# Performance work log

Measured on AMD Instinct MI355X. Metric: run time of the kernel, lower is better.

Reference implementation:

```python
import jax, jax.numpy as jnp
import numpy as np

D = 1024
H = 16
DK = D // H


def apply_rope(x):
    # x: [B, H, T, dk]; interleaved-pair RoPE as in the torch source
    T, dim = x.shape[-2], x.shape[-1]
    inv_freq = 1.0 / (10000.0 ** (jnp.arange(0, dim, 2, dtype=x.dtype) / dim))  # [dk/2]
    pos = jnp.arange(T, dtype=x.dtype)
    sinusoid = pos[:, None] * inv_freq[None, :]  # [T, dk/2]
    sin, cos = jnp.sin(sinusoid), jnp.cos(sinusoid)
    x1, x2 = x[..., ::2], x[..., 1::2]
    rot = jnp.stack([x1 * cos - x2 * sin, x1 * sin + x2 * cos], axis=-1)
    return rot.reshape(x.shape)


def setup_inputs() -> dict:
    key = jax.random.key(0)
    k1, k2, k3, k4, k5 = jax.random.split(key, 5)
    B, T = 2, 2048
    s = 1.0 / np.sqrt(D)
    return {
        "x": jax.random.normal(k1, (B, T, D), dtype=jnp.float32),
        "W_qkv": jax.random.normal(k2, (D, 3 * D), dtype=jnp.float32) * s,
        "b_qkv": jnp.zeros((3 * D,), dtype=jnp.float32),
        "W_out": jax.random.normal(k3, (D, D), dtype=jnp.float32) * s,
        "b_out": jnp.zeros((D,), dtype=jnp.float32),
    }


def reference(x, W_qkv, b_qkv, W_out, b_out):
    B, T, C = x.shape
    qkv = x @ W_qkv + b_qkv  # [B, T, 3D]
    qkv = qkv.reshape(B, T, 3, H, DK).transpose(2, 0, 3, 1, 4)  # [3, B, H, T, dk]
    q, k, v = qkv[0], qkv[1], qkv[2]
    q, k = apply_rope(q), apply_rope(k)
    scores = jnp.einsum("bhtd,bhsd->bhts", q, k) / jnp.sqrt(jnp.asarray(DK, x.dtype))
    causal = jnp.tril(jnp.ones((T, T), dtype=bool))
    scores = jnp.where(causal, scores, jnp.asarray(-1e9, x.dtype))
    probs = jax.nn.softmax(scores, axis=-1)
    attn = jnp.einsum("bhts,bhsd->bhtd", probs, v)  # [B, H, T, dk]
    out = attn.transpose(0, 2, 1, 3).reshape(B, T, C)  # b h t d -> b t (h d)
    return out @ W_out + b_out
```

## Files before the change

### kernel.cpp

```cpp
#include <hip/hip_runtime.h>
#include <math.h>

#define DMODEL 1024
#define NHEAD  16
#define HDK    64
#define BATCH  2
#define SEQ    2048
#define MROWS  (BATCH*SEQ)
#define NQKV   (3*DMODEL)
#define LOG2_10000 13.287712379549449f
#define INV2PI 0.15915494309189535f
#define SCALE_LOG2E 0.1803368801111137f
#define M_FIX 8.0f

typedef __attribute__((ext_vector_type(8))) short bf16x8;
typedef __attribute__((ext_vector_type(4))) short s16x4;
typedef __attribute__((ext_vector_type(4))) float f32x4;

__device__ __forceinline__ short f2bf(float f) {
    union { float f; unsigned u; } v; v.f = f;
    unsigned r = v.u + 0x7fffu + ((v.u >> 16) & 1u);
    return (short)(r >> 16);
}

__device__ __forceinline__ float fast_exp2(float x) {
#if __has_builtin(__builtin_amdgcn_exp2f)
    return __builtin_amdgcn_exp2f(x);
#else
    return exp2f(x);
#endif
}

__device__ __forceinline__ void gld_lds16(const short* g, short* l) {
    __builtin_amdgcn_global_load_lds(
        (const __attribute__((address_space(1))) void*)g,
        (__attribute__((address_space(3))) void*)l, 16, 0, 0);
}

__global__ __launch_bounds__(256) void prep_kernel(
    const float* __restrict__ x, const float* __restrict__ wqkv,
    const float* __restrict__ wout,
    short* __restrict__ xb, short* __restrict__ wqkv_t, short* __restrict__ wout_t)
{
    __shared__ short tile[32][33];
    const int tid = threadIdx.x;
    if (blockIdx.x < 2048) {
        const int i = (blockIdx.x * 256 + tid) * 8;
        float4 a = *(const float4*)(x + i);
        float4 b = *(const float4*)(x + i + 4);
        bf16x8 o;
        o[0] = f2bf(a.x); o[1] = f2bf(a.y); o[2] = f2bf(a.z); o[3] = f2bf(a.w);
        o[4] = f2bf(b.x); o[5] = f2bf(b.y); o[6] = f2bf(b.z); o[7] = f2bf(b.w);
        *(bf16x8*)(xb + i) = o;
        return;
    }
    const int bx = blockIdx.x - 2048;
    int nx = bx & 127;
    const int ky = bx >> 7;
    const float* in; short* out; int N;
    if (nx < 96) { in = wqkv; out = wqkv_t; N = NQKV; }
    else         { in = wout; out = wout_t; N = DMODEL; nx -= 96; }
    const int tx = tid & 31, ty = tid >> 5;
    const int n0 = nx * 32, k0 = ky * 32;
    #pragma unroll
    for (int i = 0; i < 32; i += 8)
        tile[ty + i][tx] = f2bf(in[(size_t)(k0 + ty + i) * N + n0 + tx]);
    __syncthreads();
    #pragma unroll
    for (int i = 0; i < 32; i += 8)
        out[(size_t)(n0 + ty + i) * DMODEL + k0 + tx] = tile[tx][ty + i];
}

__global__ __launch_bounds__(256) void qkv_gemm_kernel(
    const short* __restrict__ xb, const short* __restrict__ Wt,
    const float* __restrict__ bias,
    short* __restrict__ qd, short* __restrict__ kd, short* __restrict__ vtb)
{
    __shared__ __align__(16) short As[2][128 * 32];
    __shared__ __align__(16) short Bs[2][128 * 32];
    const int tid = threadIdx.x;
    const int lane = tid & 63, wave = tid >> 6;
    const int wm = wave & 1, wn = wave >> 1;
    const int l15 = lane & 15, quad = lane >> 4;
    const int n0 = blockIdx.x * 128, m0 = blockIdx.y * 128;
    const int srow = lane >> 2, sc = lane & 3;
    const int scp = sc ^ ((srow >> 1) & 3);
    const int rdx = (l15 >> 1) & 3;

    const short* gA1 = xb + (size_t)(m0 + wave * 32 + srow) * DMODEL + scp * 8;
    const short* gA2 = gA1 + (size_t)16 * DMODEL;
    const short* gB1 = Wt + (size_t)(n0 + wave * 32 + srow) * DMODEL + scp * 8;
    const short* gB2 = gB1 + (size_t)16 * DMODEL;
    const int lofsA1 = (wave * 32) * 32;
    const int lofsA2 = (wave * 32 + 16) * 32;

    f32x4 zero = {0.f, 0.f, 0.f, 0.f};
    f32x4 acc[4][4];
    #pragma unroll
    for (int i = 0; i < 4; ++i)
        #pragma unroll
        for (int j = 0; j < 4; ++j) acc[i][j] = zero;

    gld_lds16(gA1, As[0] + lofsA1);
    gld_lds16(gA2, As[0] + lofsA2);
    gld_lds16(gB1, Bs[0] + lofsA1);
    gld_lds16(gB2, Bs[0] + lofsA2);
    __syncthreads();

    for (int k = 0; k < DMODEL / 32; ++k) {
        const int cur = k & 1;
        if (k + 1 < DMODEL / 32) {
            const int kn = (k + 1) * 32;
            gld_lds16(gA1 + kn, As[cur ^ 1] + lofsA1);
            gld_lds16(gA2 + kn, As[cur ^ 1] + lofsA2);
            gld_lds16(gB1 + kn, Bs[cur ^ 1] + lofsA1);
            gld_lds16(gB2 + kn, Bs[cur ^ 1] + lofsA2);
        }
        bf16x8 af[4], bfr[4];
        #pragma unroll
        for (int i = 0; i < 4; ++i)
            af[i] = *(const bf16x8*)&As[cur][(wm * 64 + i * 16 + l15) * 32 + (quad ^ rdx) * 8];
        #pragma unroll
        for (int j = 0; j < 4; ++j)
            bfr[j] = *(const bf16x8*)&Bs[cur][(wn * 64 + j * 16 + l15) * 32 + (quad ^ rdx) * 8];
        #pragma unroll
        for (int i = 0; i < 4; ++i)
            #pragma unroll
            for (int j = 0; j < 4; ++j)
                acc[i][j] = __builtin_amdgcn_mfma_f32_16x16x32_bf16(af[i], bfr[j], acc[i][j], 0, 0, 0);
        __syncthreads();
    }

    const int which = n0 >> 10;
    float biasv[4], invf[4];
    int hh[4], dd[4];
    #pragma unroll
    for (int j = 0; j < 4; ++j) {
        const int n = n0 + wn * 64 + j * 16 + l15;
        biasv[j] = bias[n];
        hh[j] = (n & 1023) >> 6;
        dd[j] = n & 63;
        invf[j] = INV2PI * exp2f(-((float)(dd[j] & ~1) / 64.f) * LOG2_10000);
    }
    #pragma unroll
    for (int i = 0; i < 4; ++i) {
        const int mb = m0 + wm * 64 + i * 16 + quad * 4;
        const int b = mb >> 11, tb = mb & (SEQ - 1);
        if (which < 2) {
            #pragma unroll
            for (int j = 0; j < 4; ++j) {
                #pragma unroll
                for (int r = 0; r < 4; ++r) {
                    const int t = tb + r;
                    float val = acc[i][j][r] + biasv[j];
                    const float rev = (float)t * invf[j];
                    const float fr = rev - floorf(rev);
                    const float s = __builtin_amdgcn_sinf(fr);
                    const float c = __builtin_amdgcn_cosf(fr);
                    const float partner = __shfl_xor(val, 1);
                    val = (lane & 1) ? (partner * s + val * c) : (val * c - partner * s);
                    short* dst = (which == 0) ? qd : kd;
                    dst[((size_t)(b * NHEAD + hh[j]) * SEQ + t) * HDK + dd[j]] = f2bf(val);
                }
            }
        } else {
            #pragma unroll
            for (int j = 0; j < 4; ++j) {
                s16x4 sv;
                #pragma unroll
                for (int r = 0; r < 4; ++r)
                    sv[r] = f2bf(acc[i][j][r] + biasv[j]);
                *(s16x4*)&vtb[((size_t)(b * NHEAD + hh[j]) * HDK + dd[j]) * SEQ + tb] = sv;
            }
        }
    }
}

__global__ __launch_bounds__(512) void attn_mfma_kernel(
    const short* __restrict__ qd, const short* __restrict__ kd,
    const short* __restrict__ vt, short* __restrict__ od)
{
    __shared__ __align__(16) short Ks[2][2][64 * 32];
    __shared__ __align__(16) short Vs[2][2][64 * 32];
    __shared__ __align__(16) short Ps[8][16][64];
    const int tid = threadIdx.x, lane = tid & 63, w = tid >> 6;
    const int l15 = lane & 15, quad = lane >> 4;
    const int par = w >> 2;
    const int ws = w & 3;
    const int id = (int)blockIdx.x;
    const int c = id & 7, kblk = id >> 3;
    const int qt = 31 - (kblk & 31);
    const int jj = kblk >> 5;
    const int hb = c + 8 * jj;
    const int h = hb & 15, b = hb >> 4;
    const size_t base = ((size_t)(b * NHEAD + h)) * SEQ * HDK;
    const int stid = tid & 255;
    const int hi = tid >> 8;
    const int srow = stid >> 2, sc = stid & 3;
    const int lofs = srow * 32 + (sc ^ ((srow >> 1) & 3)) * 8;
    const int rdx = (l15 >> 1) & 3;
    f32x4 zero = {0.f, 0.f, 0.f, 0.f};

    const short* kp = kd + base + (size_t)(hi * 64 + srow) * HDK + sc * 8;
    const short* vp = vt + base + (size_t)srow * SEQ + hi * 64 + sc * 8;

    const int q0 = qt * 64;
    bf16x8 qf[2];
    {
        const short* qrow = qd + base + (size_t)(q0 + ws * 16 + l15) * HDK;
        qf[0] = *(const bf16x8*)(qrow + quad * 8);
        qf[1] = *(const bf16x8*)(qrow + 32 + quad * 8);
    }
    float l_acc[4] = {0.f, 0.f, 0.f, 0.f};
    f32x4 o[4];
    #pragma unroll
    for (int j = 0; j < 4; ++j) o[j] = zero;

    const int nkt = qt + 1;
    const int npair = (nkt + 1) >> 1;

    bf16x8 rk[2], rv[2];
    rk[0] = *(const bf16x8*)kp; rk[1] = *(const bf16x8*)(kp + 32);
    rv[0] = *(const bf16x8*)vp; rv[1] = *(const bf16x8*)(vp + 32);

    for (int p = 0; p < npair; ++p) {
        __syncthreads();
        *(bf16x8*)&Ks[hi][0][lofs] = rk[0];
        *(bf16x8*)&Ks[hi][1][lofs] = rk[1];
        *(bf16x8*)&Vs[hi][0][lofs] = rv[0];
        *(bf16x8*)&Vs[hi][1][lofs] = rv[1];
        __syncthreads();
        if (p + 1 < npair) {
            const int sn = (2 * p + 2) * 64;
            const short* kn = kp + (size_t)sn * HDK;
            const short* vn = vp + sn;
            rk[0] = *(const bf16x8*)kn; rk[1] = *(const bf16x8*)(kn + 32);
            rv[0] = *(const bf16x8*)vn; rv[1] = *(const bf16x8*)(vn + 32);
        }

        const int kt = 2 * p + par;
        if (kt < nkt) {
            f32x4 sacc[4];
            #pragma unroll
            for (int j = 0; j < 4; ++j) {
                const int ro = (j * 16 + l15) * 32 + ((quad ^ rdx)) * 8;
                bf16x8 kf0 = *(const bf16x8*)&Ks[par][0][ro];
                bf16x8 kf1 = *(const bf16x8*)&Ks[par][1][ro];
                sacc[j] = __builtin_amdgcn_mfma_f32_16x16x32_bf16(qf[0], kf0, zero, 0, 0, 0);
                sacc[j] = __builtin_amdgcn_mfma_f32_16x16x32_bf16(qf[1], kf1, sacc[j], 0, 0, 0);
            }
            if (kt == nkt - 1) {
                const int s0 = kt * 64;
                #pragma unroll
                for (int j = 0; j < 4; ++j) {
                    const int scol = s0 + j * 16 + l15;
                    #pragma unroll
                    for (int r = 0; r < 4; ++r) {
                        const int trow = q0 + ws * 16 + quad * 4 + r;
                        const float sv = sacc[j][r] * SCALE_LOG2E - M_FIX;
                        const float pv = (scol > trow) ? 0.f : fast_exp2(sv);
                        l_acc[r] += pv;
                        const int pr = quad * 4 + r;
                        const int sw = (j * 2 + (l15 >> 3)) ^ (pr & 7);
                        Ps[w][pr][sw * 8 + (l15 & 7)] = f2bf(pv);
                    }
                }
            } else {
                #pragma unroll
                for (int j = 0; j < 4; ++j)
                    #pragma unroll
                    for (int r = 0; r < 4; ++r) {
                        const float pv = fast_exp2(sacc[j][r] * SCALE_LOG2E - M_FIX);
                        l_acc[r] += pv;
                        const int pr = quad * 4 + r;
                        const int sw = (j * 2 + (l15 >> 3)) ^ (pr & 7);
                        Ps[w][pr][sw * 8 + (l15 & 7)] = f2bf(pv);
                    }
            }
            bf16x8 pf0 = *(const bf16x8*)&Ps[w][l15][(quad ^ (l15 & 7)) * 8];
            bf16x8 pf1 = *(const bf16x8*)&Ps[w][l15][((4 + quad) ^ (l15 & 7)) * 8];
            #pragma unroll
            for (int j = 0; j < 4; ++j) {
                const int ro = (j * 16 + l15) * 32 + ((quad ^ rdx)) * 8;
                bf16x8 vf0 = *(const bf16x8*)&Vs[par][0][ro];
                bf16x8 vf1 = *(const bf16x8*)&Vs[par][1][ro];
                o[j] = __builtin_amdgcn_mfma_f32_16x16x32_bf16(pf0, vf0, o[j], 0, 0, 0);
                o[j] = __builtin_amdgcn_mfma_f32_16x16x32_bf16(pf1, vf1, o[j], 0, 0, 0);
            }
        }
    }

    __syncthreads();
    float* ob = (float*)&Ks[0][0][0];
    float* lb = (float*)&Vs[0][0][0];
    if (par == 1) {
        const int bi = (ws * 64 + lane) * 16;
        #pragma unroll
        for (int j = 0; j < 4; ++j)
            #pragma unroll
            for (int r = 0; r < 4; ++r) ob[bi + j * 4 + r] = o[j][r];
        const int li = (ws * 64 + lane) * 4;
        #pragma unroll
        for (int r = 0; r < 4; ++r) lb[li + r] = l_acc[r];
    }
    __syncthreads();
    if (par == 0) {
        const int bi = (ws * 64 + lane) * 16;
        #pragma unroll
        for (int j = 0; j < 4; ++j)
            #pragma unroll
            for (int r = 0; r < 4; ++r) o[j][r] += ob[bi + j * 4 + r];
        const int li = (ws * 64 + lane) * 4;
        #pragma unroll
        for (int r = 0; r < 4; ++r) l_acc[r] += lb[li + r];

        #pragma unroll
        for (int r = 0; r < 4; ++r) {
            float sr = l_acc[r];
            #pragma unroll
            for (int off = 1; off < 16; off <<= 1) sr += __shfl_xor(sr, off);
            l_acc[r] = sr;
        }
        #pragma unroll
        for (int r = 0; r < 4; ++r) {
            const float inv = 1.f / l_acc[r];
            const int t = q0 + ws * 16 + quad * 4 + r;
            #pragma unroll
            for (int j = 0; j < 4; ++j)
                od[((size_t)(b * SEQ + t) * NHEAD + h) * HDK + j * 16 + l15] =
                    f2bf(o[j][r] * inv);
        }
    }
}

__global__ __launch_bounds__(256) void out_gemm_kernel(
    const short* __restrict__ Ab, const short* __restrict__ Wt,
    const float* __restrict__ bias, float* __restrict__ out)
{
    __shared__ __align__(16) short As[2][128 * 32];
    __shared__ __align__(16) short Bs[2][64 * 32];
    const int tid = threadIdx.x;
    const int lane = tid & 63, wave = tid >> 6;
    const int wm = wave & 1, wn = wave >> 1;
    const int l15 = lane & 15, quad = lane >> 4;
    const int n0 = blockIdx.x * 64, m0 = blockIdx.y * 128;
    const int srow = lane >> 2, sc = lane & 3;
    const int scp = sc ^ ((srow >> 1) & 3);
    const int rdx = (l15 >> 1) & 3;

    const short* gA1 = Ab + (size_t)(m0 + wave * 32 + srow) * DMODEL + scp * 8;
    const short* gA2 = gA1 + (size_t)16 * DMODEL;
    const short* gB1 = Wt + (size_t)(n0 + wave * 16 + srow) * DMODEL + scp * 8;
    const int lofsA1 = (wave * 32) * 32;
    const int lofsA2 = (wave * 32 + 16) * 32;
    const int lofsB  = (wave * 16) * 32;

    f32x4 zero = {0.f, 0.f, 0.f, 0.f};
    f32x4 acc[4][2];
    #pragma unroll
    for (int i = 0; i < 4; ++i)
        #pragma unroll
        for (int j = 0; j < 2; ++j) acc[i][j] = zero;

    gld_lds16(gA1, As[0] + lofsA1);
    gld_lds16(gA2, As[0] + lofsA2);
    gld_lds16(gB1, Bs[0] + lofsB);
    __syncthreads();

    for (int k = 0; k < DMODEL / 32; ++k) {
        const int cur = k & 1;
        if (k + 1 < DMODEL / 32) {
            const int kn = (k + 1) * 32;
            gld_lds16(gA1 + kn, As[cur ^ 1] + lofsA1);
            gld_lds16(gA2 + kn, As[cur ^ 1] + lofsA2);
            gld_lds16(gB1 + kn, Bs[cur ^ 1] + lofsB);
        }
        bf16x8 af[4], bfr[2];
        #pragma unroll
        for (int i = 0; i < 4; ++i)
            af[i] = *(const bf16x8*)&As[cur][(wm * 64 + i * 16 + l15) * 32 + (quad ^ rdx) * 8];
        #pragma unroll
        for (int j = 0; j < 2; ++j)
            bfr[j] = *(const bf16x8*)&Bs[cur][(wn * 32 + j * 16 + l15) * 32 + (quad ^ rdx) * 8];
        #pragma unroll
        for (int i = 0; i < 4; ++i)
            #pragma unroll
            for (int j = 0; j < 2; ++j)
                acc[i][j] = __builtin_amdgcn_mfma_f32_16x16x32_bf16(af[i], bfr[j], acc[i][j], 0, 0, 0);
        __syncthreads();
    }

    #pragma unroll
    for (int j = 0; j < 2; ++j) {
        const int n = n0 + wn * 32 + j * 16 + l15;
        const float bv = bias[n];
        #pragma unroll
        for (int i = 0; i < 4; ++i)
            #pragma unroll
            for (int r = 0; r < 4; ++r) {
                const int m = m0 + wm * 64 + i * 16 + quad * 4 + r;
                out[(size_t)m * DMODEL + n] = acc[i][j][r] + bv;
            }
    }
}

extern "C" void kernel_launch(void* const* d_in, const int* in_sizes, int n_in,
                              void* d_out, int out_size, void* d_ws, size_t ws_size,
                              hipStream_t stream) {
    const float* x    = (const float*)d_in[0];
    const float* Wqkv = (const float*)d_in[1];
    const float* bqkv = (const float*)d_in[2];
    const float* Wout = (const float*)d_in[3];
    const float* bout = (const float*)d_in[4];
    float* out = (float*)d_out;

    short* ws = (short*)d_ws;
    short* xb     = ws;
    short* wqkv_t = xb + (size_t)4 * 1024 * 1024;
    short* wout_t = wqkv_t + (size_t)3 * 1024 * 1024;
    short* qd     = wout_t + (size_t)1024 * 1024;
    short* kd     = qd + (size_t)4 * 1024 * 1024;
    short* vtb    = kd + (size_t)4 * 1024 * 1024;
    short* attn   = vtb + (size_t)4 * 1024 * 1024;

    prep_kernel<<<2048 + 4096, 256, 0, stream>>>(x, Wqkv, Wout, xb, wqkv_t, wout_t);

    qkv_gemm_kernel<<<dim3(NQKV / 128, MROWS / 128), 256, 0, stream>>>(
        xb, wqkv_t, bqkv, qd, kd, vtb);

    attn_mfma_kernel<<<1024, 512, 0, stream>>>(qd, kd, vtb, attn);

    out_gemm_kernel<<<dim3(DMODEL / 64, MROWS / 128), 256, 0, stream>>>(
        attn, wout_t, bout, out);
}
```

Measured before the change: 185.7 us.

## Transpose QK^T MFMA so each lane owns one query row, packed bf16 P stores

Swaps the MFMA operand order so the score tile comes out transposed, letting each lane hold four consecutive key columns for one query row. P values are then converted with hardware packed bf16 conversion and stored as 8-byte vectors instead of scalar shorts, and the row-sum becomes a single scalar reduced with two shuffles plus a small LDS exchange. Block-to-tile mapping also changes so neighbouring blocks share a query-tile index across heads. The aim is to cut LDS store instructions and software rounding ALU work in the softmax section. The cost is inline asm and a new swizzle scheme that must stay conflict-free.

Result: faster. 176.0 us (-5.2%).

```diff
diff --git a/kernel.cpp b/kernel.cpp
--- a/kernel.cpp
+++ b/kernel.cpp
@@ -16,6 +16,7 @@
 typedef __attribute__((ext_vector_type(8))) short bf16x8;
 typedef __attribute__((ext_vector_type(4))) short s16x4;
 typedef __attribute__((ext_vector_type(4))) float f32x4;
+typedef __attribute__((ext_vector_type(2))) unsigned int u32x2;
 
 __device__ __forceinline__ short f2bf(float f) {
     union { float f; unsigned u; } v; v.f = f;
@@ -182,15 +183,15 @@
 {
     __shared__ __align__(16) short Ks[2][2][64 * 32];
     __shared__ __align__(16) short Vs[2][2][64 * 32];
-    __shared__ __align__(16) short Ps[8][16][64];
+    __shared__ __align__(16) short Ps[8][16 * 64];
     const int tid = threadIdx.x, lane = tid & 63, w = tid >> 6;
     const int l15 = lane & 15, quad = lane >> 4;
     const int par = w >> 2;
     const int ws = w & 3;
     const int id = (int)blockIdx.x;
-    const int c = id & 7, kblk = id >> 3;
-    const int qt = 31 - (kblk & 31);
-    const int jj = kblk >> 5;
+    const int c = id & 7, g = id >> 3;
+    const int qt = 31 - (g >> 2);
+    const int jj = g & 3;
     const int hb = c + 8 * jj;
     const int h = hb & 15, b = hb >> 4;
     const size_t base = ((size_t)(b * NHEAD + h)) * SEQ * HDK;
@@ -199,25 +200,28 @@
     const int srow = stid >> 2, sc = stid & 3;
     const int lofs = srow * 32 + (sc ^ ((srow >> 1) & 3)) * 8;
     const int rdx = (l15 >> 1) & 3;
+    const int pmask = (l15 & 3) << 2;
     f32x4 zero = {0.f, 0.f, 0.f, 0.f};
 
     const short* kp = kd + base + (size_t)(hi * 64 + srow) * HDK + sc * 8;
     const short* vp = vt + base + (size_t)srow * SEQ + hi * 64 + sc * 8;
 
     const int q0 = qt * 64;
+    const int trow = q0 + ws * 16 + l15;
     bf16x8 qf[2];
     {
-        const short* qrow = qd + base + (size_t)(q0 + ws * 16 + l15) * HDK;
+        const short* qrow = qd + base + (size_t)trow * HDK;
         qf[0] = *(const bf16x8*)(qrow + quad * 8);
         qf[1] = *(const bf16x8*)(qrow + 32 + quad * 8);
     }
-    float l_acc[4] = {0.f, 0.f, 0.f, 0.f};
+    float l_acc = 0.f;
     f32x4 o[4];
     #pragma unroll
     for (int j = 0; j < 4; ++j) o[j] = zero;
 
     const int nkt = qt + 1;
     const int npair = (nkt + 1) >> 1;
+    short* myPs = &Ps[w][0];
 
     bf16x8 rk[2], rv[2];
     rk[0] = *(const bf16x8*)kp; rk[1] = *(const bf16x8*)(kp + 32);
@@ -243,45 +247,53 @@
             f32x4 sacc[4];
             #pragma unroll
             for (int j = 0; j < 4; ++j) {
-                const int ro = (j * 16 + l15) * 32 + ((quad ^ rdx)) * 8;
+                const int ro = (j * 16 + l15) * 32 + (quad ^ rdx) * 8;
                 bf16x8 kf0 = *(const bf16x8*)&Ks[par][0][ro];
                 bf16x8 kf1 = *(const bf16x8*)&Ks[par][1][ro];
-                sacc[j] = __builtin_amdgcn_mfma_f32_16x16x32_bf16(qf[0], kf0, zero, 0, 0, 0);
-                sacc[j] = __builtin_amdgcn_mfma_f32_16x16x32_bf16(qf[1], kf1, sacc[j], 0, 0, 0);
+                sacc[j] = __builtin_amdgcn_mfma_f32_16x16x32_bf16(kf0, qf[0], zero, 0, 0, 0);
+                sacc[j] = __builtin_amdgcn_mfma_f32_16x16x32_bf16(kf1, qf[1], sacc[j], 0, 0, 0);
             }
             if (kt == nkt - 1) {
                 const int s0 = kt * 64;
                 #pragma unroll
                 for (int j = 0; j < 4; ++j) {
-                    const int scol = s0 + j * 16 + l15;
+                    float pv[4];
                     #pragma unroll
                     for (int r = 0; r < 4; ++r) {
-                        const int trow = q0 + ws * 16 + quad * 4 + r;
+                        const int scol = s0 + j * 16 + quad * 4 + r;
                         const float sv = sacc[j][r] * SCALE_LOG2E - M_FIX;
-                        const float pv = (scol > trow) ? 0.f : fast_exp2(sv);
-                        l_acc[r] += pv;
-                        const int pr = quad * 4 + r;
-                        const int sw = (j * 2 + (l15 >> 3)) ^ (pr & 7);
-                        Ps[w][pr][sw * 8 + (l15 & 7)] = f2bf(pv);
+                        pv[r] = (scol > trow) ? 0.f : fast_exp2(sv);
+                        l_acc += pv[r];
                     }
+                    unsigned pk0, pk1;
+                    asm("v_cvt_pk_bf16_f32 %0, %1, %2" : "=v"(pk0) : "v"(pv[0]), "v"(pv[1]));
+                    asm("v_cvt_pk_bf16_f32 %0, %1, %2" : "=v"(pk1) : "v"(pv[2]), "v"(pv[3]));
+                    const int cc = (j * 4 + quad) ^ pmask;
+                    u32x2 pkv = {pk0, pk1};
+                    *(u32x2*)&myPs[l15 * 64 + cc * 4] = pkv;
                 }
             } else {
                 #pragma unroll
-                for (int j = 0; j < 4; ++j)
+                for (int j = 0; j < 4; ++j) {
+                    float pv[4];
                     #pragma unroll
                     for (int r = 0; r < 4; ++r) {
-                        const float pv = fast_exp2(sacc[j][r] * SCALE_LOG2E - M_FIX);
-                        l_acc[r] += pv;
-                        const int pr = quad * 4 + r;
-                        const int sw = (j * 2 + (l15 >> 3)) ^ (pr & 7);
-                        Ps[w][pr][sw * 8 + (l15 & 7)] = f2bf(pv);
+                        pv[r] = fast_exp2(sacc[j][r] * SCALE_LOG2E - M_FIX);
+                        l_acc += pv[r];
                     }
-            }
-            bf16x8 pf0 = *(const bf16x8*)&Ps[w][l15][(quad ^ (l15 & 7)) * 8];
-            bf16x8 pf1 = *(const bf16x8*)&Ps[w][l15][((4 + quad) ^ (l15 & 7)) * 8];
+                    unsigned pk0, pk1;
+                    asm("v_cvt_pk_bf16_f32 %0, %1, %2" : "=v"(pk0) : "v"(pv[0]), "v"(pv[1]));
+                    asm("v_cvt_pk_bf16_f32 %0, %1, %2" : "=v"(pk1) : "v"(pv[2]), "v"(pv[3]));
+                    const int cc = (j * 4 + quad) ^ pmask;
+                    u32x2 pkv = {pk0, pk1};
+                    *(u32x2*)&myPs[l15 * 64 + cc * 4] = pkv;
+                }
+            }
+            bf16x8 pf0 = *(const bf16x8*)&myPs[l15 * 64 + ((quad * 2) ^ pmask) * 4];
+            bf16x8 pf1 = *(const bf16x8*)&myPs[l15 * 64 + ((8 + quad * 2) ^ pmask) * 4];
             #pragma unroll
             for (int j = 0; j < 4; ++j) {
-                const int ro = (j * 16 + l15) * 32 + ((quad ^ rdx)) * 8;
+                const int ro = (j * 16 + l15) * 32 + (quad ^ rdx) * 8;
                 bf16x8 vf0 = *(const bf16x8*)&Vs[par][0][ro];
                 bf16x8 vf1 = *(const bf16x8*)&Vs[par][1][ro];
                 o[j] = __builtin_amdgcn_mfma_f32_16x16x32_bf16(pf0, vf0, o[j], 0, 0, 0);
@@ -290,18 +302,20 @@
         }
     }
 
+    float sr = l_acc;
+    sr += __shfl_xor(sr, 16);
+    sr += __shfl_xor(sr, 32);
+
     __syncthreads();
-    float* ob = (float*)&Ks[0][0][0];
-    float* lb = (float*)&Vs[0][0][0];
+    float* ob   = (float*)&Ks[0][0][0];
+    float* lbuf = (float*)&Vs[0][0][0];
+    lbuf[w * 16 + l15] = sr;
     if (par == 1) {
         const int bi = (ws * 64 + lane) * 16;
         #pragma unroll
         for (int j = 0; j < 4; ++j)
             #pragma unroll
             for (int r = 0; r < 4; ++r) ob[bi + j * 4 + r] = o[j][r];
-        const int li = (ws * 64 + lane) * 4;
-        #pragma unroll
-        for (int r = 0; r < 4; ++r) lb[li + r] = l_acc[r];
     }
     __syncthreads();
     if (par == 0) {
@@ -310,21 +324,13 @@
         for (int j = 0; j < 4; ++j)
             #pragma unroll
             for (int r = 0; r < 4; ++r) o[j][r] += ob[bi + j * 4 + r];
-        const int li = (ws * 64 + lane) * 4;
-        #pragma unroll
-        for (int r = 0; r < 4; ++r) l_acc[r] += lb[li + r];
 
         #pragma unroll
         for (int r = 0; r < 4; ++r) {
-            float sr = l_acc[r];
-            #pragma unroll
-            for (int off = 1; off < 16; off <<= 1) sr += __shfl_xor(sr, off);
-            l_acc[r] = sr;
-        }
-        #pragma unroll
-        for (int r = 0; r < 4; ++r) {
-            const float inv = 1.f / l_acc[r];
-            const int t = q0 + ws * 16 + quad * 4 + r;
+            const int qq = quad * 4 + r;
+            const float lt = lbuf[ws * 16 + qq] + lbuf[(ws + 4) * 16 + qq];
+            const float inv = 1.f / lt;
+            const int t = q0 + ws * 16 + qq;
             #pragma unroll
             for (int j = 0; j < 4; ++j)
                 od[((size_t)(b * SEQ + t) * NHEAD + h) * HDK + j * 16 + l15] =
```
